# Optimization experiments

Hardware: AMD Instinct MI355X
Metric: run time of the kernel (lower is better)

## Reference

```python
import jax, jax.numpy as jnp
import numpy as np

N_NODES = 100000
N_EDGES = 600000
D = 128
NUM_RELS = 200


def setup_inputs() -> dict:
    key = jax.random.key(0)
    ks = jax.random.split(key, 12)
    s = 1.0 / np.sqrt(D)
    return {
        "h": jax.random.normal(ks[0], (N_NODES, D), jnp.float32),
        "prev_h": jax.random.normal(ks[1], (N_NODES, D), jnp.float32),
        "emb_rel": jax.random.normal(ks[2], (NUM_RELS, D), jnp.float32),
        "norm": jax.random.uniform(ks[3], (N_NODES, 1), jnp.float32),
        "weight_neighbor": jax.random.normal(ks[4], (D, D), jnp.float32) * s,
        "loop_weight": jax.random.normal(ks[5], (D, D), jnp.float32) * s,
        "evolve_loop_weight": jax.random.normal(ks[6], (D, D), jnp.float32) * s,
        "skip_connect_weight": jax.random.normal(ks[7], (D, D), jnp.float32) * s,
        "skip_connect_bias": jnp.zeros((D,), jnp.float32),
        "src": jax.random.randint(ks[8], (N_EDGES,), 0, N_NODES, jnp.int64),
        "dst": jax.random.randint(ks[9], (N_EDGES,), 0, N_NODES, jnp.int64),
        "etype": jax.random.randint(ks[10], (N_EDGES,), 0, NUM_RELS, jnp.int64),
    }


def reference(h, prev_h, emb_rel, norm, weight_neighbor, loop_weight,
              evolve_loop_weight, skip_connect_weight, skip_connect_bias,
              src, dst, etype):
    n = h.shape[0]
    # self-loop message: nodes with in-degree > 0 use loop_weight, else evolve_loop_weight
    in_deg = jax.ops.segment_sum(jnp.ones_like(dst, dtype=jnp.float32), dst,
                                 num_segments=n)  # [N]
    loop_message = jnp.where(in_deg[:, None] > 0,
                             h @ loop_weight,
                             h @ evolve_loop_weight)  # [N, D]
    # skip gate from previous layer hidden state
    skip_weight = jax.nn.sigmoid(prev_h @ skip_connect_weight + skip_connect_bias)
    # msg_func: gather src node feats + relation embedding, per-edge GEMM
    msg = (h[src] + emb_rel[etype]) @ weight_neighbor  # [E, D]
    # fn.sum scatter aggregation, then apply_func: multiply by node norm
    agg = jax.ops.segment_sum(msg, dst, num_segments=n)  # [N, D]
    node_repr = agg * norm
    # skip_connect (prev_h non-empty) + self_loop branch
    node_repr = node_repr + loop_message
    node_repr = skip_weight * node_repr + (1.0 - skip_weight) * prev_h
    # activation
    return jax.nn.relu(node_repr)
```

## Files before the change

kernel.cpp:

```cpp
#include <hip/hip_runtime.h>

#define DD 128

typedef __attribute__((ext_vector_type(8))) short short8;
typedef __attribute__((ext_vector_type(4))) float f32x4;
typedef __attribute__((ext_vector_type(4))) int i32x4;

__device__ __forceinline__ unsigned short f2bf(float f) {
    union { float f; unsigned int i; } c; c.f = f;
    unsigned int x = c.i;
    return (unsigned short)((x + 0x7fffu + ((x >> 16) & 1u)) >> 16);
}
__device__ __forceinline__ float bfu(unsigned short u) {
    union { unsigned int i; float f; } c; c.i = ((unsigned int)u) << 16; return c.f;
}
__device__ __forceinline__ void gload_lds16(const void* g, void* l) {
    __builtin_amdgcn_global_load_lds(
        (const __attribute__((address_space(1))) unsigned int*)g,
        (__attribute__((address_space(3))) unsigned int*)l, 16, 0, 0);
}
__device__ __forceinline__ int idx_at(const int* p, int e, int is64) {
    return is64 ? p[2 * e] : p[e];
}
__device__ __forceinline__ int block_is64(const int* dst, int nE, int* s_flag) {
    if (threadIdx.x == 0) *s_flag = 0;
    __syncthreads();
    int w = 2 * (int)threadIdx.x + 1;
    if (threadIdx.x < 128 && w < nE && dst[w] != 0) atomicOr(s_flag, 1);
    __syncthreads();
    return !*s_flag;
}

__global__ __launch_bounds__(256) void prep_k(
    const float* __restrict__ h, const float* __restrict__ prevh,
    const float* __restrict__ W0, const float* __restrict__ W1,
    const float* __restrict__ W2, const float* __restrict__ emb,
    const int* __restrict__ dst,
    unsigned short* __restrict__ hB, char* __restrict__ aggP,
    unsigned short* __restrict__ embB, unsigned short* __restrict__ Wt,
    int* __restrict__ deg, int nN, int nEmbEl, int nE) {
    int tid = threadIdx.x;
    int bid = blockIdx.x;
    int totalH = nN * DD;
    int nConvH = (totalH + 2047) / 2048;
    if (bid < 2 * nConvH) {
        int which = bid >= nConvH;
        int base = (which ? bid - nConvH : bid) * 2048 + tid * 8;
        const float* S = which ? prevh : h;
        if (base + 8 <= totalH) {
            f32x4 x0 = *(const f32x4*)(S + base);
            f32x4 x1 = *(const f32x4*)(S + base + 4);
            short8 p;
            #pragma unroll
            for (int j = 0; j < 4; ++j) {
                p[j]     = (short)f2bf(x0[j]);
                p[4 + j] = (short)f2bf(x1[j]);
            }
            if (which) {
                int row = base >> 7, col = base & 127;
                *(short8*)(aggP + (size_t)row * 512 + 256 + col * 2) = p;
            } else {
                *(short8*)(hB + base) = p;
            }
        } else {
            for (int j = base; j < totalH; ++j) {
                unsigned short v = f2bf(S[j]);
                if (which) *(unsigned short*)(aggP + (size_t)(j >> 7) * 512 + 256 +
                                              (j & 127) * 2) = v;
                else hB[j] = v;
            }
        }
        return;
    }
    bid -= 2 * nConvH;
    if (bid < 48) {
        const float* Ws[3] = {W0, W1, W2};
        int w = bid >> 4, chunk = bid & 15;
        unsigned short* T = Wt + w * (DD * DD);
        #pragma unroll
        for (int i = 0; i < 4; ++i) {
            int t = chunk * 1024 + i * 256 + tid;
            int n = t >> 7, k = t & 127;
            T[t] = f2bf(Ws[w][k * DD + n]);
        }
        return;
    }
    bid -= 48;
    int nEmbB = (nEmbEl + 2047) / 2048;
    if (bid < nEmbB) {
        int base = bid * 2048 + tid * 8;
        if (base + 8 <= nEmbEl) {
            f32x4 x0 = *(const f32x4*)(emb + base);
            f32x4 x1 = *(const f32x4*)(emb + base + 4);
            short8 p;
            #pragma unroll
            for (int j = 0; j < 4; ++j) {
                p[j]     = (short)f2bf(x0[j]);
                p[4 + j] = (short)f2bf(x1[j]);
            }
            *(short8*)(embB + base) = p;
        } else {
            for (int j = base; j < nEmbEl; ++j) embB[j] = f2bf(emb[j]);
        }
        return;
    }
    bid -= nEmbB;
    __shared__ int s_flag;
    int is64 = block_is64(dst, nE, &s_flag);
    int e = bid * 256 + tid;
    if (e < nE) atomicAdd(deg + idx_at(dst, e, is64), 1);
}

__global__ __launch_bounds__(1024) void scan1_k(const int* deg, int* off, int* bsum,
                                                int nN) {
    __shared__ int s[1024];
    int t = threadIdx.x, i = blockIdx.x * 1024 + t;
    int v = (i < nN) ? deg[i] : 0;
    s[t] = v;
    __syncthreads();
    for (int d = 1; d < 1024; d <<= 1) {
        int x = (t >= d) ? s[t - d] : 0;
        __syncthreads();
        s[t] += x;
        __syncthreads();
    }
    if (i < nN) off[i] = s[t] - v;
    if (t == 1023) bsum[blockIdx.x] = s[1023];
}

__global__ __launch_bounds__(1024) void scan23_k(const int* bsum, int* off,
                                                 int* cursor, int nN, int nB) {
    __shared__ int s[1024];
    int t = threadIdx.x;
    s[t] = (t < nB) ? bsum[t] : 0;
    __syncthreads();
    for (int d = 1; d < 1024; d <<= 1) {
        int x = (t >= d) ? s[t - d] : 0;
        __syncthreads();
        s[t] += x;
        __syncthreads();
    }
    int base = (blockIdx.x == 0) ? 0 : s[blockIdx.x - 1];
    int i = blockIdx.x * 1024 + t;
    if (i < nN) {
        int o = off[i] + base;
        off[i] = o;
        cursor[i] = o;
    }
}

__global__ __launch_bounds__(256) void sort_k(const int* src, const int* dst,
                                              const int* et, int nE,
                                              int* cursor, unsigned int* edges) {
    __shared__ int s_flag;
    int is64 = block_is64(dst, nE, &s_flag);
    int e = blockIdx.x * 256 + threadIdx.x;
    if (e >= nE) return;
    int d = idx_at(dst, e, is64);
    int pos = atomicAdd(cursor + d, 1);
    edges[pos] = (unsigned int)idx_at(src, e, is64) |
                 ((unsigned int)idx_at(et, e, is64) << 17);
}

__global__ __launch_bounds__(256) void gather_k(
    const unsigned short* __restrict__ hB, const unsigned short* __restrict__ embB,
    const unsigned int* __restrict__ edges, const int* __restrict__ off,
    const int* __restrict__ deg, const float* __restrict__ normv,
    char* __restrict__ aggP, int nN) {
    int lane = threadIdx.x & 63;
    int v = blockIdx.x * 4 + (threadIdx.x >> 6);
    if (v >= nN) return;
    int slot = lane >> 4, l16 = lane & 15;
    int b = off[v], n = deg[v];
    float a[8] = {0.f, 0.f, 0.f, 0.f, 0.f, 0.f, 0.f, 0.f};
    for (int base = 0; base < n; base += 8) {
        int m0 = base + slot, m1 = base + 4 + slot;
        bool v0 = m0 < n, v1 = m1 < n;
        unsigned int w0 = 0, w1 = 0;
        if (v0) w0 = edges[b + m0];
        if (v1) w1 = edges[b + m1];
        short8 hv0, rv0, hv1, rv1;
        if (v0) {
            hv0 = *(const short8*)(hB + (size_t)(w0 & 0x1FFFFu) * DD + l16 * 8);
            rv0 = *(const short8*)(embB + (size_t)(w0 >> 17) * DD + l16 * 8);
        }
        if (v1) {
            hv1 = *(const short8*)(hB + (size_t)(w1 & 0x1FFFFu) * DD + l16 * 8);
            rv1 = *(const short8*)(embB + (size_t)(w1 >> 17) * DD + l16 * 8);
        }
        if (v0) {
            #pragma unroll
            for (int j = 0; j < 8; ++j)
                a[j] += bfu((unsigned short)hv0[j]) + bfu((unsigned short)rv0[j]);
        }
        if (v1) {
            #pragma unroll
            for (int j = 0; j < 8; ++j)
                a[j] += bfu((unsigned short)hv1[j]) + bfu((unsigned short)rv1[j]);
        }
    }
    #pragma unroll
    for (int j = 0; j < 8; ++j) {
        a[j] += __shfl_xor(a[j], 16);
        a[j] += __shfl_xor(a[j], 32);
    }
    if (slot == 0) {
        float nm = normv[v];
        short8 p;
        #pragma unroll
        for (int j = 0; j < 8; ++j) p[j] = (short)f2bf(a[j] * nm);
        *(short8*)(aggP + (size_t)v * 512 + l16 * 16) = p;
    }
}

__global__ __launch_bounds__(256, 3) void fused_k(
    const unsigned short* __restrict__ hB,
    const float* __restrict__ bias,
    const char* __restrict__ aggP,
    const unsigned short* __restrict__ Wt,
    float* __restrict__ out, int nN) {
    __shared__ unsigned short lds[3 * 64 * 128];
    const int lane = threadIdx.x & 63;
    const int wv = threadIdx.x >> 6;
    const int q = lane >> 4, cl = lane & 15;
    const int node_base = blockIdx.x * 64;
    const int ncb = wv * 32;

    {
        int r0 = lane >> 4;
        int c  = lane & 15;
        #pragma unroll
        for (int it = 0; it < 4; ++it) {
            int r = it * 16 + wv * 4 + r0;
            int row = node_base + r; if (row > nN - 1) row = nN - 1;
            int sw = (c ^ (r & 15)) << 4;
            const char* gA = aggP + (size_t)row * 512 + sw;
            const char* gP = aggP + (size_t)row * 512 + 256 + sw;
            const char* gH = (const char*)hB + (size_t)row * 256 + sw;
            char* base = (char*)lds + (it * 16 + wv * 4) * 256;
            gload_lds16(gA, base);
            gload_lds16(gH, base + 16384);
            gload_lds16(gP, base + 32768);
        }
    }
    __syncthreads();

    const unsigned short* lA = lds;
    const unsigned short* lH = lds + 64 * 128;
    const unsigned short* lP = lds + 2 * 64 * 128;

    f32x4 accM[4][2], accG[4][2];
    #pragma unroll
    for (int mt = 0; mt < 4; ++mt)
        #pragma unroll
        for (int nt = 0; nt < 2; ++nt) {
            accM[mt][nt] = (f32x4){0.f, 0.f, 0.f, 0.f};
            accG[mt][nt] = (f32x4){0.f, 0.f, 0.f, 0.f};
        }

    #pragma unroll
    for (int ks = 0; ks < 4; ++ks) {
        short8 bn[2], bl[2], bs[2];
        #pragma unroll
        for (int nt = 0; nt < 2; ++nt) {
            int n = (ncb + nt * 16 + cl) * DD + ks * 32 + q * 8;
            bn[nt] = *(const short8*)(Wt + n);
            bl[nt] = *(const short8*)(Wt + DD * DD + n);
            bs[nt] = *(const short8*)(Wt + 2 * DD * DD + n);
        }
        int swz = ((ks * 4 + q) ^ cl) << 3;
        #pragma unroll
        for (int mt = 0; mt < 4; ++mt) {
            int off = (mt * 16 + cl) * 128 + swz;
            short8 aA = *(const short8*)(lA + off);
            short8 aH = *(const short8*)(lH + off);
            short8 aP = *(const short8*)(lP + off);
            #pragma unroll
            for (int nt = 0; nt < 2; ++nt) {
                accM[mt][nt] = __builtin_amdgcn_mfma_f32_16x16x32_bf16(
                    aA, bn[nt], accM[mt][nt], 0, 0, 0);
                accM[mt][nt] = __builtin_amdgcn_mfma_f32_16x16x32_bf16(
                    aH, bl[nt], accM[mt][nt], 0, 0, 0);
                accG[mt][nt] = __builtin_amdgcn_mfma_f32_16x16x32_bf16(
                    aP, bs[nt], accG[mt][nt], 0, 0, 0);
            }
        }
    }

    float b0 = bias[ncb + cl], b1 = bias[ncb + 16 + cl];

    #pragma unroll
    for (int mt = 0; mt < 4; ++mt) {
        #pragma unroll
        for (int r = 0; r < 4; ++r) {
            int nrow = mt * 16 + q * 4 + r;
            int node = node_base + nrow;
            if (node >= nN) continue;
            #pragma unroll
            for (int nt = 0; nt < 2; ++nt) {
                int col = ncb + nt * 16 + cl;
                float pv = bfu(lP[nrow * 128 +
                                  ((((col >> 3) ^ (nrow & 15)) << 3) | (col & 7))]);
                float sg = 1.0f / (1.0f + __expf(-(accG[mt][nt][r] + (nt ? b1 : b0))));
                float o  = sg * accM[mt][nt][r] + (1.0f - sg) * pv;
                out[(size_t)node * DD + col] = (o > 0.f ? o : 0.f);
            }
        }
    }
}

__global__ __launch_bounds__(256) void fix_k(
    const float* __restrict__ h, const float* __restrict__ prevh,
    const float* __restrict__ bias, const float* __restrict__ We,
    const float* __restrict__ Wsk, const int* __restrict__ deg,
    float* __restrict__ out, int nN, int chunk) {
    __shared__ int list[256];
    __shared__ int cnt;
    __shared__ float hrow[DD], prow[DD], res[2][DD];
    int tid = threadIdx.x;
    int base = blockIdx.x * chunk;
    for (int c = base; c < base + chunk && c < nN; c += 256) {
        if (tid == 0) cnt = 0;
        __syncthreads();
        int v = c + tid;
        if (v < nN && v < base + chunk && deg[v] == 0)
            list[atomicAdd(&cnt, 1)] = v;
        __syncthreads();
        int m = cnt;
        for (int i = 0; i < m; ++i) {
            int node = list[i];
            if (tid < DD) hrow[tid] = h[(size_t)node * DD + tid];
            else prow[tid - DD] = prevh[(size_t)node * DD + tid - DD];
            __syncthreads();
            int col = tid & (DD - 1);
            int half = tid >> 7;
            const float* W = half ? Wsk : We;
            const float* x = half ? prow : hrow;
            float s = 0.f;
            for (int k = 0; k < DD; ++k) s += x[k] * W[k * DD + col];
            res[half][col] = s;
            __syncthreads();
            if (tid < DD) {
                float sg = 1.0f / (1.0f + __expf(-(res[1][col] + bias[col])));
                float o  = sg * res[0][col] + (1.0f - sg) * prow[col];
                out[(size_t)node * DD + col] = (o > 0.f ? o : 0.f);
            }
            __syncthreads();
        }
        __syncthreads();
    }
}

extern "C" void kernel_launch(void* const* d_in, const int* in_sizes, int n_in,
                              void* d_out, int out_size, void* d_ws, size_t ws_size,
                              hipStream_t stream) {
    const float* h     = (const float*)d_in[0];
    const float* prevh = (const float*)d_in[1];
    const float* emb   = (const float*)d_in[2];
    const float* normv = (const float*)d_in[3];
    const float* Wn    = (const float*)d_in[4];
    const float* Wl    = (const float*)d_in[5];
    const float* We    = (const float*)d_in[6];
    const float* Wsk   = (const float*)d_in[7];
    const float* bias  = (const float*)d_in[8];
    const int* src   = (const int*)d_in[9];
    const int* dst   = (const int*)d_in[10];
    const int* etype = (const int*)d_in[11];

    int nN = in_sizes[3];
    int nE = in_sizes[9];
    int nEmbEl = in_sizes[2];

    char* w = (char*)d_ws;
    size_t o = 0;
    unsigned short* Wt = (unsigned short*)(w + o);  o += 3 * DD * DD * 2;
    unsigned short* embB = (unsigned short*)(w + o); o += ((size_t)nEmbEl * 2 + 255) & ~(size_t)255;
    int* deg    = (int*)(w + o);  o += ((size_t)nN * 4 + 15) & ~(size_t)15;
    int* offA   = (int*)(w + o);  o += ((size_t)nN * 4 + 15) & ~(size_t)15;
    int* cursor = (int*)(w + o);  o += ((size_t)nN * 4 + 15) & ~(size_t)15;
    int* bsum   = (int*)(w + o);  o += 4096;
    unsigned int* edges = (unsigned int*)(w + o); o += ((size_t)nE * 4 + 15) & ~(size_t)15;
    unsigned short* hB = (unsigned short*)(w + o);

    int nConvH = (nN * DD + 2047) / 2048;
    int nEmbB  = (nEmbEl + 2047) / 2048;
    int nHistB = (nE + 255) / 256;
    int nB = (nN + 1023) / 1024;

    hipMemsetAsync(deg, 0, (size_t)nN * sizeof(int), stream);
    prep_k<<<2 * nConvH + 48 + nEmbB + nHistB, 256, 0, stream>>>(
        h, prevh, Wn, Wl, Wsk, emb, dst, hB, (char*)d_out, embB, Wt, deg,
        nN, nEmbEl, nE);
    scan1_k<<<nB, 1024, 0, stream>>>(deg, offA, bsum, nN);
    scan23_k<<<nB, 1024, 0, stream>>>(bsum, offA, cursor, nN, nB);
    sort_k<<<(nE + 255) / 256, 256, 0, stream>>>(src, dst, etype, nE, cursor, edges);
    gather_k<<<(nN + 3) / 4, 256, 0, stream>>>(hB, embB, edges, offA, deg, normv,
                                               (char*)d_out, nN);
    fused_k<<<(nN + 63) / 64, 256, 0, stream>>>(hB, bias, (const char*)d_out, Wt,
                                                (float*)d_out, nN);
    int fgrid = 256;
    int chunk = ((nN + fgrid * 256 - 1) / (fgrid * 256)) * 256;
    fix_k<<<fgrid, 256, 0, stream>>>(h, prevh, bias, We, Wsk, deg, (float*)d_out,
                                     nN, chunk);
    (void)ws_size; (void)n_in; (void)out_size;
}
```

Baseline: 322.2 us.

## Fuse prev_h bf16 conversion into fused kernel and reorder prep blocks

Result: no change. 318.0 us (-1.3%).

```diff
diff --git a/kernel.cpp b/kernel.cpp
--- a/kernel.cpp
+++ b/kernel.cpp
@@ -32,47 +32,73 @@
 }
 
 __global__ __launch_bounds__(256) void prep_k(
-    const float* __restrict__ h, const float* __restrict__ prevh,
+    const float* __restrict__ h,
     const float* __restrict__ W0, const float* __restrict__ W1,
     const float* __restrict__ W2, const float* __restrict__ emb,
     const int* __restrict__ dst,
-    unsigned short* __restrict__ hB, char* __restrict__ aggP,
+    unsigned short* __restrict__ hB,
     unsigned short* __restrict__ embB, unsigned short* __restrict__ Wt,
     int* __restrict__ deg, int nN, int nEmbEl, int nE) {
     int tid = threadIdx.x;
     int bid = blockIdx.x;
+    int nHistB = (nE + 1023) / 1024;
+    if (bid < nHistB) {
+        __shared__ int s_flag;
+        int is64 = block_is64(dst, nE, &s_flag);
+        int e0 = bid * 1024 + tid * 4;
+        #pragma unroll
+        for (int j = 0; j < 4; ++j) {
+            int e = e0 + j;
+            if (e < nE) atomicAdd(deg + idx_at(dst, e, is64), 1);
+        }
+        return;
+    }
+    bid -= nHistB;
     int totalH = nN * DD;
-    int nConvH = (totalH + 2047) / 2048;
-    if (bid < 2 * nConvH) {
-        int which = bid >= nConvH;
-        int base = (which ? bid - nConvH : bid) * 2048 + tid * 8;
-        const float* S = which ? prevh : h;
-        if (base + 8 <= totalH) {
-            f32x4 x0 = *(const f32x4*)(S + base);
-            f32x4 x1 = *(const f32x4*)(S + base + 4);
-            short8 p;
-            #pragma unroll
-            for (int j = 0; j < 4; ++j) {
-                p[j]     = (short)f2bf(x0[j]);
-                p[4 + j] = (short)f2bf(x1[j]);
-            }
-            if (which) {
-                int row = base >> 7, col = base & 127;
-                *(short8*)(aggP + (size_t)row * 512 + 256 + col * 2) = p;
-            } else {
-                *(short8*)(hB + base) = p;
+    int nConvH = (totalH + 8191) / 8192;
+    if (bid < nConvH) {
+        int base0 = bid * 8192;
+        if (base0 + 8192 <= totalH) {
+            int base = base0 + tid * 8;
+            f32x4 x[4][2];
+            #pragma unroll
+            for (int i = 0; i < 4; ++i) {
+                x[i][0] = *(const f32x4*)(h + base + i * 2048);
+                x[i][1] = *(const f32x4*)(h + base + i * 2048 + 4);
+            }
+            #pragma unroll
+            for (int i = 0; i < 4; ++i) {
+                short8 p;
+                #pragma unroll
+                for (int j = 0; j < 4; ++j) {
+                    p[j]     = (short)f2bf(x[i][0][j]);
+                    p[4 + j] = (short)f2bf(x[i][1][j]);
+                }
+                *(short8*)(hB + base + i * 2048) = p;
             }
         } else {
-            for (int j = base; j < totalH; ++j) {
-                unsigned short v = f2bf(S[j]);
-                if (which) *(unsigned short*)(aggP + (size_t)(j >> 7) * 512 + 256 +
-                                              (j & 127) * 2) = v;
-                else hB[j] = v;
+            #pragma unroll
+            for (int i = 0; i < 4; ++i) {
+                int b2 = base0 + i * 2048 + tid * 8;
+                if (b2 + 8 <= totalH) {
+                    f32x4 x0 = *(const f32x4*)(h + b2);
+                    f32x4 x1 = *(const f32x4*)(h + b2 + 4);
+                    short8 p;
+                    #pragma unroll
+                    for (int j = 0; j < 4; ++j) {
+                        p[j]     = (short)f2bf(x0[j]);
+                        p[4 + j] = (short)f2bf(x1[j]);
+                    }
+                    *(short8*)(hB + b2) = p;
+                } else {
+                    for (int j = b2; j < totalH && j < b2 + 8; ++j)
+                        hB[j] = f2bf(h[j]);
+                }
             }
         }
         return;
     }
-    bid -= 2 * nConvH;
+    bid -= nConvH;
     if (bid < 48) {
         const float* Ws[3] = {W0, W1, W2};
         int w = bid >> 4, chunk = bid & 15;
@@ -86,29 +112,20 @@
         return;
     }
     bid -= 48;
-    int nEmbB = (nEmbEl + 2047) / 2048;
-    if (bid < nEmbB) {
-        int base = bid * 2048 + tid * 8;
-        if (base + 8 <= nEmbEl) {
-            f32x4 x0 = *(const f32x4*)(emb + base);
-            f32x4 x1 = *(const f32x4*)(emb + base + 4);
-            short8 p;
-            #pragma unroll
-            for (int j = 0; j < 4; ++j) {
-                p[j]     = (short)f2bf(x0[j]);
-                p[4 + j] = (short)f2bf(x1[j]);
-            }
-            *(short8*)(embB + base) = p;
-        } else {
-            for (int j = base; j < nEmbEl; ++j) embB[j] = f2bf(emb[j]);
-        }
-        return;
-    }
-    bid -= nEmbB;
-    __shared__ int s_flag;
-    int is64 = block_is64(dst, nE, &s_flag);
-    int e = bid * 256 + tid;
-    if (e < nE) atomicAdd(deg + idx_at(dst, e, is64), 1);
+    int base = bid * 2048 + tid * 8;
+    if (base + 8 <= nEmbEl) {
+        f32x4 x0 = *(const f32x4*)(emb + base);
+        f32x4 x1 = *(const f32x4*)(emb + base + 4);
+        short8 p;
+        #pragma unroll
+        for (int j = 0; j < 4; ++j) {
+            p[j]     = (short)f2bf(x0[j]);
+            p[4 + j] = (short)f2bf(x1[j]);
+        }
+        *(short8*)(embB + base) = p;
+    } else {
+        for (int j = base; j < nEmbEl; ++j) embB[j] = f2bf(emb[j]);
+    }
 }
 
 __global__ __launch_bounds__(1024) void scan1_k(const int* deg, int* off, int* bsum,
@@ -215,6 +232,7 @@
 
 __global__ __launch_bounds__(256, 3) void fused_k(
     const unsigned short* __restrict__ hB,
+    const float* __restrict__ prevh,
     const float* __restrict__ bias,
     const char* __restrict__ aggP,
     const unsigned short* __restrict__ Wt,
@@ -234,13 +252,36 @@
             int r = it * 16 + wv * 4 + r0;
             int row = node_base + r; if (row > nN - 1) row = nN - 1;
             int sw = (c ^ (r & 15)) << 4;
-            const char* gA = aggP + (size_t)row * 512 + sw;
-            const char* gP = aggP + (size_t)row * 512 + 256 + sw;
-            const char* gH = (const char*)hB + (size_t)row * 256 + sw;
             char* base = (char*)lds + (it * 16 + wv * 4) * 256;
-            gload_lds16(gA, base);
-            gload_lds16(gH, base + 16384);
-            gload_lds16(gP, base + 32768);
+            gload_lds16(aggP + (size_t)row * 512 + sw, base);
+            gload_lds16((const char*)hB + (size_t)row * 256 + sw, base + 16384);
+        }
+    }
+    {
+        f32x4 t0[4], t1[4];
+        #pragma unroll
+        for (int it = 0; it < 4; ++it) {
+            int pos = it * 512 + lane * 8;
+            int row = pos >> 7;
+            int col = pos & 127;
+            int node = node_base + wv * 16 + row;
+            if (node > nN - 1) node = nN - 1;
+            const float* g = prevh + (size_t)node * DD + col;
+            t0[it] = *(const f32x4*)g;
+            t1[it] = *(const f32x4*)(g + 4);
+        }
+        #pragma unroll
+        for (int it = 0; it < 4; ++it) {
+            int pos = it * 512 + lane * 8;
+            int r = wv * 16 + (pos >> 7);
+            int c = (pos & 127) >> 3;
+            short8 p;
+            #pragma unroll
+            for (int j = 0; j < 4; ++j) {
+                p[j]     = (short)f2bf(t0[it][j]);
+                p[4 + j] = (short)f2bf(t1[it][j]);
+            }
+            *(short8*)((char*)lds + 32768 + r * 256 + ((c ^ (r & 15)) << 4)) = p;
         }
     }
     __syncthreads();
@@ -382,22 +423,22 @@
     unsigned int* edges = (unsigned int*)(w + o); o += ((size_t)nE * 4 + 15) & ~(size_t)15;
     unsigned short* hB = (unsigned short*)(w + o);
 
-    int nConvH = (nN * DD + 2047) / 2048;
+    int totalH = nN * DD;
+    int nConvH = (totalH + 8191) / 8192;
     int nEmbB  = (nEmbEl + 2047) / 2048;
-    int nHistB = (nE + 255) / 256;
+    int nHistB = (nE + 1023) / 1024;
     int nB = (nN + 1023) / 1024;
 
     hipMemsetAsync(deg, 0, (size_t)nN * sizeof(int), stream);
-    prep_k<<<2 * nConvH + 48 + nEmbB + nHistB, 256, 0, stream>>>(
-        h, prevh, Wn, Wl, Wsk, emb, dst, hB, (char*)d_out, embB, Wt, deg,
-        nN, nEmbEl, nE);
+    prep_k<<<nHistB + nConvH + 48 + nEmbB, 256, 0, stream>>>(
+        h, Wn, Wl, Wsk, emb, dst, hB, embB, Wt, deg, nN, nEmbEl, nE);
     scan1_k<<<nB, 1024, 0, stream>>>(deg, offA, bsum, nN);
     scan23_k<<<nB, 1024, 0, stream>>>(bsum, offA, cursor, nN, nB);
     sort_k<<<(nE + 255) / 256, 256, 0, stream>>>(src, dst, etype, nE, cursor, edges);
     gather_k<<<(nN + 3) / 4, 256, 0, stream>>>(hB, embB, edges, offA, deg, normv,
                                                (char*)d_out, nN);
-    fused_k<<<(nN + 63) / 64, 256, 0, stream>>>(hB, bias, (const char*)d_out, Wt,
-                                                (float*)d_out, nN);
+    fused_k<<<(nN + 63) / 64, 256, 0, stream>>>(hB, prevh, bias, (const char*)d_out,
+                                                Wt, (float*)d_out, nN);
     int fgrid = 256;
     int chunk = ((nN + fgrid * 256 - 1) / (fgrid * 256)) * 256;
     fix_k<<<fgrid, 256, 0, stream>>>(h, prevh, bias, We, Wsk, deg, (float*)d_out,
```
